# Kernel optimization log

Hardware: AMD Instinct MI355X
Metric: run time of the kernel (lower is better)

Reference implementation:

```python
import jax, jax.numpy as jnp
import numpy as np

EPS = 1e-12  # matches torch F.normalize eps
TEMPERATURE = 1.0


def _l2_normalize(x):
    n = jnp.sqrt(jnp.sum(x * x, axis=-1, keepdims=True))
    return x / jnp.maximum(n, EPS)


def setup_inputs() -> dict:
    key = jax.random.key(0)
    k1, k2 = jax.random.split(key)
    B, L, D, V = 2, 2048, 1024, 32000
    embeddings = jax.random.normal(k1, (B, L, D), dtype=jnp.float32)
    vocab_embeddings = jax.random.normal(k2, (V, D), dtype=jnp.float32)
    return {"embeddings": embeddings, "vocab_embeddings": vocab_embeddings, "k": 8}


def reference(embeddings, vocab_embeddings, k):
    """Soft KNN routing: cosine similarity -> top-k -> temperature softmax
    scattered into a full (B, L, V) probability distribution, plus hard
    argmax token ids (forward())."""
    B, L, D = embeddings.shape
    V = vocab_embeddings.shape[0]
    q = _l2_normalize(embeddings.reshape(-1, D))          # (N, D)
    vocab = _l2_normalize(vocab_embeddings)               # (V, D)
    sims = q @ vocab.T                                    # (N, V) cosine similarities
    topk_sim, topk_idx = jax.lax.top_k(sims, k)           # (N, k)
    probs_k = jax.nn.softmax(topk_sim / TEMPERATURE, axis=-1)
    N = q.shape[0]
    probs = jnp.zeros((N, V), dtype=probs_k.dtype)
    probs = probs.at[jnp.arange(N)[:, None], topk_idx].set(probs_k)
    probs = probs.reshape(B, L, V)                        # forward_soft output
    token_ids = topk_idx[:, 0].reshape(B, L)              # forward() hard routing (k=1)
    return probs, token_ids
```

## Files before the change

### kernel.cpp

```cpp
#include <hip/hip_runtime.h>
#include <math.h>

typedef unsigned short u16;
typedef unsigned int u32;
typedef float f32x16 __attribute__((ext_vector_type(16)));
typedef short bf16x8 __attribute__((ext_vector_type(8)));
typedef u16 u16x4 __attribute__((ext_vector_type(4)));

static constexpr int N = 4096;
static constexpr int D = 1024;
static constexpr int V = 32000;
static constexpr int K = 8;
static constexpr int BM = 128, BN = 128, BK = 64;
static constexpr int NTILES = V / BN;
static constexpr int NG = 32;
static constexpr int NCAND = NG * K;
static constexpr int T16 = 16;
static constexpr int CPL = NCAND / 64;
static constexpr int GRID = NG * (N / BM);
static constexpr u32 PSENT = 0x00800000u;

static constexpr size_t OUT_PROB_BYTES = (size_t)N * V * 4;
static constexpr size_t CAND_OFS = 83886080;
static constexpr size_t ZOFS = CAND_OFS + (size_t)N * NCAND * 4;
static constexpr size_t NZ4 = (OUT_PROB_BYTES - ZOFS) / 16;

static_assert(N % BM == 0 && V % BN == 0, "tiling");
static_assert(ZOFS % 16 == 0, "align");
static_assert(NZ4 == (size_t)104 * GRID * 256, "zero quota");

__device__ __forceinline__ u16 f2bf(float f) {
  u32 u = __float_as_uint(f);
  return (u16)((u + 0x7fffu + ((u >> 16) & 1u)) >> 16);
}
__device__ __forceinline__ u32 flipbits(float v) {
  u32 u = __float_as_uint(v);
  return u ^ (((u32)((int)u >> 31)) | 0x80000000u);
}
__device__ __forceinline__ float unpackval(u32 p) {
  u32 s = p | 1023u;
  u32 u = (s & 0x80000000u) ? (s ^ 0x80000000u) : ~s;
  return __uint_as_float(u);
}
__device__ __forceinline__ void insert8(u32 pv[K], u32 x) {
  if (x <= pv[K - 1]) return;
  bool g[K];
#pragma unroll
  for (int j = 0; j < K; ++j) g[j] = x > pv[j];
#pragma unroll
  for (int j = K - 1; j >= 1; --j)
    pv[j] = g[j - 1] ? pv[j - 1] : (g[j] ? x : pv[j]);
  if (g[0]) pv[0] = x;
}

__global__ void zero_kernel(float4* __restrict__ p, int n4) {
  int i = blockIdx.x * blockDim.x + threadIdx.x;
  int stride = gridDim.x * blockDim.x;
  float4 z = make_float4(0.f, 0.f, 0.f, 0.f);
  for (; i < n4; i += stride) p[i] = z;
}

__global__ void normcvt_kernel(const float* __restrict__ x, float* __restrict__ inv,
                               u16* __restrict__ o) {
  int row = blockIdx.x;
  const float4* xr = reinterpret_cast<const float4*>(x + (size_t)row * D);
  float4 v = xr[threadIdx.x];
  float ss = v.x * v.x + v.y * v.y + v.z * v.z + v.w * v.w;
#pragma unroll
  for (int off = 32; off > 0; off >>= 1) ss += __shfl_down(ss, off, 64);
  __shared__ float wsum[4];
  if ((threadIdx.x & 63) == 0) wsum[threadIdx.x >> 6] = ss;
  __syncthreads();
  __shared__ float s_inv;
  if (threadIdx.x == 0) {
    float t = wsum[0] + wsum[1] + wsum[2] + wsum[3];
    float iv = 1.0f / fmaxf(sqrtf(t), 1e-12f);
    inv[row] = iv;
    s_inv = iv;
  }
  __syncthreads();
  float s = s_inv;
  u16x4 r;
  r[0] = f2bf(v.x * s); r[1] = f2bf(v.y * s); r[2] = f2bf(v.z * s); r[3] = f2bf(v.w * s);
  *reinterpret_cast<u16x4*>(o + (size_t)row * D + threadIdx.x * 4) = r;
}

__global__ __launch_bounds__(256, 4)
void simtopk_kernel(const u16* __restrict__ qn, const u16* __restrict__ vn,
                    u32* __restrict__ cand, float4* __restrict__ zout) {
  __shared__ __align__(16) u16 sh[2 * BM * BK];

  u16* a_sh = sh;
  u16* b_sh = sh + BM * BK;

  const int tid = threadIdx.x;
  const int bid = blockIdx.x;
  const int u = bid >> 3;
  const int rb = u & 31;
  const int grp = (bid & 7) * 4 + (u >> 5);
  const int t0 = (grp * NTILES) >> 5;
  const int t1 = ((grp + 1) * NTILES) >> 5;
  const int rbase = rb * BM;
  const int wid = tid >> 6, l = tid & 63;
  const int wr = wid >> 1, wc = wid & 1;
  const int h = l >> 5, lid = l & 31;
  const int sr = l >> 3;
  const int sk = (((l & 7) ^ (l >> 3)) << 3);

  const float4 zf4 = make_float4(0.f, 0.f, 0.f, 0.f);

  u32 pv[2][K];
#pragma unroll
  for (int n = 0; n < 2; ++n)
#pragma unroll
    for (int j = 0; j < K; ++j) pv[n][j] = PSENT;
  float tminf[2] = {-3.0e38f, -3.0e38f};

  for (int ti = t0; ti < t1; ++ti) {
    const int cb = (ti - t0) * BN;
    f32x16 acc[2][2];
#pragma unroll
    for (int m = 0; m < 2; ++m)
#pragma unroll
      for (int n = 0; n < 2; ++n)
#pragma unroll
        for (int r = 0; r < 16; ++r) acc[m][n][r] = 0.f;

    for (int kk = 0; kk < D / BK; ++kk) {
      __syncthreads();
      {
        int it = (ti - t0) * 16 + kk;
        size_t g = (size_t)it * (GRID * 256) + (size_t)bid * 256 + tid;
        if (g < NZ4) zout[g] = zf4;
      }
      const int kbase = kk * BK;
#pragma unroll
      for (int c = 0; c < 4; ++c) {
        int r = wid * 32 + c * 8 + sr;
        const u16* gs = qn + (size_t)(rbase + r) * D + kbase + sk;
        __builtin_amdgcn_global_load_lds((const __attribute__((address_space(1))) void*)gs,
            (__attribute__((address_space(3))) void*)(a_sh + wid * 2048 + c * 512), 16, 0, 0);
      }
#pragma unroll
      for (int c = 0; c < 4; ++c) {
        int r = wid * 32 + c * 8 + sr;
        const u16* gs = vn + (size_t)(ti * BN + r) * D + kbase + sk;
        __builtin_amdgcn_global_load_lds((const __attribute__((address_space(1))) void*)gs,
            (__attribute__((address_space(3))) void*)(b_sh + wid * 2048 + c * 512), 16, 0, 0);
      }
      __syncthreads();
      __builtin_amdgcn_s_setprio(1);
#pragma unroll
      for (int t = 0; t < 4; ++t) {
        const int ch = t * 2 + h;
        bf16x8 vf[2], qf[2];
#pragma unroll
        for (int m = 0; m < 2; ++m) {
          int row = wr * 64 + m * 32 + lid;
          vf[m] = *reinterpret_cast<const bf16x8*>(b_sh + row * BK + ((ch ^ (row & 7)) << 3));
        }
#pragma unroll
        for (int n = 0; n < 2; ++n) {
          int row = wc * 64 + n * 32 + lid;
          qf[n] = *reinterpret_cast<const bf16x8*>(a_sh + row * BK + ((ch ^ (row & 7)) << 3));
        }
#pragma unroll
        for (int m = 0; m < 2; ++m)
#pragma unroll
          for (int n = 0; n < 2; ++n)
            acc[m][n] = __builtin_amdgcn_mfma_f32_32x32x16_bf16(vf[m], qf[n], acc[m][n], 0, 0, 0);
      }
      __builtin_amdgcn_s_setprio(0);
    }

#pragma unroll
    for (int n = 0; n < 2; ++n) {
#pragma unroll
      for (int m = 0; m < 2; ++m) {
        f32x16 a = acc[m][n];
        float x01 = fmaxf(a[0], a[1]),   x23 = fmaxf(a[2], a[3]);
        float x45 = fmaxf(a[4], a[5]),   x67 = fmaxf(a[6], a[7]);
        float x89 = fmaxf(a[8], a[9]),   xab = fmaxf(a[10], a[11]);
        float xcd = fmaxf(a[12], a[13]), xef = fmaxf(a[14], a[15]);
        float mx = fmaxf(fmaxf(fmaxf(x01, x23), fmaxf(x45, x67)),
                         fmaxf(fmaxf(x89, xab), fmaxf(xcd, xef)));
        if (mx > tminf[n]) {
          const int cidb = cb + wr * 64 + m * 32 + 4 * h;
#pragma unroll
          for (int r = 0; r < 16; ++r) {
            float v = a[r];
            if (v > tminf[n]) {
              int cid = cidb + (r & 3) + 8 * (r >> 2);
              u32 p = (flipbits(v) & 0xFFFFFC00u) | (u32)(1023 - cid);
              insert8(pv[n], p);
            }
          }
          tminf[n] = unpackval(pv[n][K - 1]);
        }
      }
    }
  }

  __syncthreads();
  u32* marr = (u32*)sh;
#pragma unroll
  for (int n = 0; n < 2; ++n)
#pragma unroll
    for (int j = 0; j < K; ++j)
      marr[((wc * 64 + n * 32 + lid) * 4 + (wr * 2 + h)) * K + j] = pv[n][j];
  __syncthreads();
  if (tid < BM) {
    u32 fv[K];
#pragma unroll
    for (int j = 0; j < K; ++j) fv[j] = PSENT;
#pragma unroll
    for (int c4 = 0; c4 < 4; ++c4)
#pragma unroll
      for (int j = 0; j < K; ++j) insert8(fv, marr[(tid * 4 + c4) * K + j]);
#pragma unroll
    for (int j = 0; j < K; ++j)
      cand[(size_t)(rbase + tid) * NCAND + grp * K + j] = fv[j];
  }
}

__global__ __launch_bounds__(256)
void rescore_kernel(const u32* __restrict__ cand,
                    const float* __restrict__ emb, const float* __restrict__ vocab,
                    const float* __restrict__ invq, const float* __restrict__ invv,
                    float* __restrict__ res_p, int* __restrict__ res_i) {
  const int tid = threadIdx.x, wid = tid >> 6, l = tid & 63;
  const int row = blockIdx.x * 4 + wid;

  float4 q[4];
#pragma unroll
  for (int t = 0; t < 4; ++t)
    q[t] = *(reinterpret_cast<const float4*>(emb + (size_t)row * D) + t * 64 + l);
  float iqr = invq[row];

  u32 pl[CPL]; int li[CPL];
#pragma unroll
  for (int t = 0; t < CPL; ++t) {
    int e = l * CPL + t;
    u32 p = cand[(size_t)row * NCAND + e];
    int grp = e >> 3;
    int tile0 = (grp * NTILES) >> 5;
    pl[t] = p;
    li[t] = tile0 * BN + 1023 - (int)(p & 1023u);
  }

  int cidx[T16];
#pragma unroll
  for (int jr = 0; jr < T16; ++jr) {
    u32 bp = pl[0]; int bi = li[0];
#pragma unroll
    for (int t = 1; t < CPL; ++t)
      if (pl[t] > bp || (pl[t] == bp && li[t] < bi)) { bp = pl[t]; bi = li[t]; }
#pragma unroll
    for (int off = 32; off > 0; off >>= 1) {
      u32 op = (u32)__shfl_xor((int)bp, off, 64); int oi = __shfl_xor(bi, off, 64);
      if (op > bp || (op == bp && oi < bi)) { bp = op; bi = oi; }
    }
    cidx[jr] = bi;
#pragma unroll
    for (int t = 0; t < CPL; ++t) if (li[t] == bi) pl[t] = 0u;
  }

  float sv[T16];
#pragma unroll
  for (int jr = 0; jr < T16; ++jr) {
    int ix = cidx[jr];
    const float4* vr = reinterpret_cast<const float4*>(vocab + (size_t)ix * D);
    float s = 0.f;
#pragma unroll
    for (int t = 0; t < 4; ++t) {
      float4 vv = vr[t * 64 + l];
      s += q[t].x * vv.x + q[t].y * vv.y + q[t].z * vv.z + q[t].w * vv.w;
    }
#pragma unroll
    for (int off = 32; off > 0; off >>= 1) s += __shfl_xor(s, off, 64);
    sv[jr] = s * iqr * invv[ix];
  }

  float pvv[K]; int pii[K];
#pragma unroll
  for (int r8 = 0; r8 < K; ++r8) {
    float bv = sv[0]; int bi = cidx[0];
#pragma unroll
    for (int jr = 1; jr < T16; ++jr)
      if (sv[jr] > bv || (sv[jr] == bv && cidx[jr] < bi)) { bv = sv[jr]; bi = cidx[jr]; }
    pvv[r8] = bv; pii[r8] = bi;
#pragma unroll
    for (int jr = 0; jr < T16; ++jr) if (cidx[jr] == bi) sv[jr] = -3.0e38f;
  }

  float m = pvv[0], sum = 0.f, e8[K];
#pragma unroll
  for (int j = 0; j < K; ++j) { e8[j] = expf(pvv[j] - m); sum += e8[j]; }
  float isum = 1.f / sum;
  if (l == 0) {
#pragma unroll
    for (int j = 0; j < K; ++j) {
      res_p[row * K + j] = e8[j] * isum;
      res_i[row * K + j] = pii[j];
    }
  }
}

__global__ void scatter_kernel(const float* __restrict__ res_p, const int* __restrict__ res_i,
                               float* __restrict__ out) {
  int row = blockIdx.x * blockDim.x + threadIdx.x;
#pragma unroll
  for (int j = 0; j < K; ++j) out[(size_t)row * V + res_i[row * K + j]] = res_p[row * K + j];
  out[(size_t)N * V + row] = (float)res_i[row * K];
}

extern "C" void kernel_launch(void* const* d_in, const int* in_sizes, int n_in,
                              void* d_out, int out_size, void* d_ws, size_t ws_size,
                              hipStream_t stream) {
  const float* emb   = (const float*)d_in[0];
  const float* vocab = (const float*)d_in[1];
  float* out = (float*)d_out;

  u16* qn = (u16*)d_out;
  u16* vn = qn + (size_t)N * D;
  u32* cand = (u32*)((char*)d_out + CAND_OFS);
  float4* ztail = (float4*)((char*)d_out + ZOFS);

  float* wsf   = (float*)d_ws;
  float* invq  = wsf;
  float* invv  = wsf + N;
  float* res_p = wsf + N + V;
  int*   res_i = (int*)(wsf + N + V + N * K);

  normcvt_kernel<<<N, 256, 0, stream>>>(emb, invq, qn);
  normcvt_kernel<<<V, 256, 0, stream>>>(vocab, invv, vn);
  simtopk_kernel<<<GRID, 256, 0, stream>>>(qn, vn, cand, ztail);
  rescore_kernel<<<N / 4, 256, 0, stream>>>(cand, emb, vocab, invq, invv, res_p, res_i);
  zero_kernel<<<2048, 256, 0, stream>>>((float4*)d_out, (int)(ZOFS / 16));
  scatter_kernel<<<N / 256, 256, 0, stream>>>(res_p, res_i, out);
}
```

Measured before the change: 535.8 us.

## Triple-buffer K-loop with async LDS loads and batch zero-fill per tile

```diff
diff --git a/kernel.cpp b/kernel.cpp
--- a/kernel.cpp
+++ b/kernel.cpp
@@ -11,7 +11,7 @@
 static constexpr int D = 1024;
 static constexpr int V = 32000;
 static constexpr int K = 8;
-static constexpr int BM = 128, BN = 128, BK = 64;
+static constexpr int BM = 128, BN = 128;
 static constexpr int NTILES = V / BN;
 static constexpr int NG = 32;
 static constexpr int NCAND = NG * K;
@@ -27,7 +27,8 @@
 
 static_assert(N % BM == 0 && V % BN == 0, "tiling");
 static_assert(ZOFS % 16 == 0, "align");
-static_assert(NZ4 == (size_t)104 * GRID * 256, "zero quota");
+static_assert((size_t)32 * 250 * 14 * 256 >= NZ4, "zero quota");
+static_assert((size_t)32 * 250 * 14 * 256 - NZ4 < NZ4, "single wrap");
 
 __device__ __forceinline__ u16 f2bf(float f) {
   u32 u = __float_as_uint(f);
@@ -85,27 +86,26 @@
   *reinterpret_cast<u16x4*>(o + (size_t)row * D + threadIdx.x * 4) = r;
 }
 
-__global__ __launch_bounds__(256, 4)
+__global__ __launch_bounds__(256, 3)
 void simtopk_kernel(const u16* __restrict__ qn, const u16* __restrict__ vn,
                     u32* __restrict__ cand, float4* __restrict__ zout) {
-  __shared__ __align__(16) u16 sh[2 * BM * BK];
-
-  u16* a_sh = sh;
-  u16* b_sh = sh + BM * BK;
+  __shared__ __align__(16) u16 sh[3 * 8192];
 
   const int tid = threadIdx.x;
   const int bid = blockIdx.x;
-  const int u = bid >> 3;
-  const int rb = u & 31;
-  const int grp = (bid & 7) * 4 + (u >> 5);
+  const int u_ = bid >> 3;
+  const int rb = u_ & 31;
+  const int grp = (bid & 7) * 4 + (u_ >> 5);
   const int t0 = (grp * NTILES) >> 5;
   const int t1 = ((grp + 1) * NTILES) >> 5;
+  const int U = (t1 - t0) * 32;
   const int rbase = rb * BM;
   const int wid = tid >> 6, l = tid & 63;
   const int wr = wid >> 1, wc = wid & 1;
   const int h = l >> 5, lid = l & 31;
-  const int sr = l >> 3;
-  const int sk = (((l & 7) ^ (l >> 3)) << 3);
+  const int sc = (((tid & 3) ^ ((tid >> 3) & 3)) << 3);
+  const int sr0 = tid >> 2;
+  const int fsw = (lid >> 1) & 3;
 
   const float4 zf4 = make_float4(0.f, 0.f, 0.f, 0.f);
 
@@ -116,63 +116,59 @@
     for (int j = 0; j < K; ++j) pv[n][j] = PSENT;
   float tminf[2] = {-3.0e38f, -3.0e38f};
 
-  for (int ti = t0; ti < t1; ++ti) {
-    const int cb = (ti - t0) * BN;
-    f32x16 acc[2][2];
-#pragma unroll
-    for (int m = 0; m < 2; ++m)
-#pragma unroll
-      for (int n = 0; n < 2; ++n)
-#pragma unroll
-        for (int r = 0; r < 16; ++r) acc[m][n][r] = 0.f;
-
-    for (int kk = 0; kk < D / BK; ++kk) {
-      __syncthreads();
-      {
-        int it = (ti - t0) * 16 + kk;
-        size_t g = (size_t)it * (GRID * 256) + (size_t)bid * 256 + tid;
-        if (g < NZ4) zout[g] = zf4;
+  f32x16 acc[2][2];
+#pragma unroll
+  for (int m = 0; m < 2; ++m)
+#pragma unroll
+    for (int n = 0; n < 2; ++n)
+#pragma unroll
+      for (int r = 0; r < 16; ++r) acc[m][n][r] = 0.f;
+
+  auto STAGE = [&](int w, int slot) {
+    const int ti = t0 + (w >> 5);
+    const int gk = (w & 31) * 32;
+    u16* ub = sh + slot * 8192;
+#pragma unroll
+    for (int s = 0; s < 2; ++s) {
+      int r = s * 64 + sr0;
+      const u16* gq = qn + (size_t)(rbase + r) * D + gk + sc;
+      __builtin_amdgcn_global_load_lds((const __attribute__((address_space(1))) void*)gq,
+          (__attribute__((address_space(3))) void*)(ub + s * 2048 + wid * 512), 16, 0, 0);
+      const u16* gv = vn + (size_t)(ti * BN + r) * D + gk + sc;
+      __builtin_amdgcn_global_load_lds((const __attribute__((address_space(1))) void*)gv,
+          (__attribute__((address_space(3))) void*)(ub + 4096 + s * 2048 + wid * 512), 16, 0, 0);
+    }
+  };
+
+  auto COMPUTE = [&](int slot) {
+    u16* ub = sh + slot * 8192;
+    __builtin_amdgcn_s_setprio(1);
+#pragma unroll
+    for (int t = 0; t < 2; ++t) {
+      const int ch = t * 2 + h;
+      const int co = (ch ^ fsw) << 3;
+      bf16x8 vf[2], qf[2];
+#pragma unroll
+      for (int m = 0; m < 2; ++m) {
+        int row = wr * 64 + m * 32 + lid;
+        vf[m] = *reinterpret_cast<const bf16x8*>(ub + 4096 + row * 32 + co);
       }
-      const int kbase = kk * BK;
-#pragma unroll
-      for (int c = 0; c < 4; ++c) {
-        int r = wid * 32 + c * 8 + sr;
-        const u16* gs = qn + (size_t)(rbase + r) * D + kbase + sk;
-        __builtin_amdgcn_global_load_lds((const __attribute__((address_space(1))) void*)gs,
-            (__attribute__((address_space(3))) void*)(a_sh + wid * 2048 + c * 512), 16, 0, 0);
+#pragma unroll
+      for (int n = 0; n < 2; ++n) {
+        int row = wc * 64 + n * 32 + lid;
+        qf[n] = *reinterpret_cast<const bf16x8*>(ub + row * 32 + co);
       }
 #pragma unroll
-      for (int c = 0; c < 4; ++c) {
-        int r = wid * 32 + c * 8 + sr;
-        const u16* gs = vn + (size_t)(ti * BN + r) * D + kbase + sk;
-        __builtin_amdgcn_global_load_lds((const __attribute__((address_space(1))) void*)gs,
-            (__attribute__((address_space(3))) void*)(b_sh + wid * 2048 + c * 512), 16, 0, 0);
-      }
-      __syncthreads();
-      __builtin_amdgcn_s_setprio(1);
-#pragma unroll
-      for (int t = 0; t < 4; ++t) {
-        const int ch = t * 2 + h;
-        bf16x8 vf[2], qf[2];
-#pragma unroll
-        for (int m = 0; m < 2; ++m) {
-          int row = wr * 64 + m * 32 + lid;
-          vf[m] = *reinterpret_cast<const bf16x8*>(b_sh + row * BK + ((ch ^ (row & 7)) << 3));
-        }
-#pragma unroll
-        for (int n = 0; n < 2; ++n) {
-          int row = wc * 64 + n * 32 + lid;
-          qf[n] = *reinterpret_cast<const bf16x8*>(a_sh + row * BK + ((ch ^ (row & 7)) << 3));
-        }
-#pragma unroll
-        for (int m = 0; m < 2; ++m)
-#pragma unroll
-          for (int n = 0; n < 2; ++n)
-            acc[m][n] = __builtin_amdgcn_mfma_f32_32x32x16_bf16(vf[m], qf[n], acc[m][n], 0, 0, 0);
-      }
-      __builtin_amdgcn_s_setprio(0);
-    }
-
+      for (int m = 0; m < 2; ++m)
+#pragma unroll
+        for (int n = 0; n < 2; ++n)
+          acc[m][n] = __builtin_amdgcn_mfma_f32_32x32x16_bf16(vf[m], qf[n], acc[m][n], 0, 0, 0);
+    }
+    __builtin_amdgcn_s_setprio(0);
+  };
+
+  auto SCAN = [&](int tt) {
+    const int cb = tt * BN;
 #pragma unroll
     for (int n = 0; n < 2; ++n) {
 #pragma unroll
@@ -199,6 +195,37 @@
         }
       }
     }
+#pragma unroll
+    for (int m = 0; m < 2; ++m)
+#pragma unroll
+      for (int n = 0; n < 2; ++n)
+#pragma unroll
+        for (int r = 0; r < 16; ++r) acc[m][n][r] = 0.f;
+  };
+
+  STAGE(0, 0);
+  STAGE(1, 1);
+  for (int w = 0; w < U; ++w) {
+    const int slot = w % 3;
+    if (w == U - 1)                        asm volatile("s_waitcnt vmcnt(0)" ::: "memory");
+    else if (w >= 32 && (w & 31) <= 1)     asm volatile("s_waitcnt vmcnt(18)" ::: "memory");
+    else                                   asm volatile("s_waitcnt vmcnt(4)" ::: "memory");
+    __builtin_amdgcn_s_barrier();
+    __builtin_amdgcn_sched_barrier(0);
+    if (w + 2 < U) STAGE(w + 2, (w + 2) % 3);
+    COMPUTE(slot);
+    asm volatile("s_waitcnt lgkmcnt(0)" ::: "memory");
+    __builtin_amdgcn_sched_barrier(0);
+    if ((w & 31) == 31) {
+      const int ti = t0 + (w >> 5);
+      size_t gbase = ((size_t)(rb * NTILES + ti) * 14) * 256 + tid;
+#pragma unroll
+      for (int j = 0; j < 14; ++j) {
+        size_t g = gbase + (size_t)j * 256;
+        zout[g < NZ4 ? g : g - NZ4] = zf4;
+      }
+      SCAN(w >> 5);
+    }
   }
 
   __syncthreads();
```

Result: slower. 606.0 us (+13.1%).

## Widen vocab tile to 256 and halve the vocab group count in simtopk

Applied to the files above, without the earlier changes.

```diff
diff --git a/kernel.cpp b/kernel.cpp
--- a/kernel.cpp
+++ b/kernel.cpp
@@ -11,13 +11,15 @@
 static constexpr int D = 1024;
 static constexpr int V = 32000;
 static constexpr int K = 8;
-static constexpr int BM = 128, BN = 128, BK = 64;
-static constexpr int NTILES = V / BN;
-static constexpr int NG = 32;
+static constexpr int BM = 128;
+static constexpr int BV = 256;
+static constexpr int BK = 64;
+static constexpr int NTILES = V / BV;
+static constexpr int NG = 16;
 static constexpr int NCAND = NG * K;
 static constexpr int T16 = 16;
 static constexpr int CPL = NCAND / 64;
-static constexpr int GRID = NG * (N / BM);
+static constexpr int GRID = (N / BM) * NG;
 static constexpr u32 PSENT = 0x00800000u;
 
 static constexpr size_t OUT_PROB_BYTES = (size_t)N * V * 4;
@@ -25,9 +27,9 @@
 static constexpr size_t ZOFS = CAND_OFS + (size_t)N * NCAND * 4;
 static constexpr size_t NZ4 = (OUT_PROB_BYTES - ZOFS) / 16;
 
-static_assert(N % BM == 0 && V % BN == 0, "tiling");
+static_assert(N % BM == 0 && V % BV == 0, "tiling");
 static_assert(ZOFS % 16 == 0, "align");
-static_assert(NZ4 == (size_t)104 * GRID * 256, "zero quota");
+static_assert(NZ4 == (size_t)209 * GRID * 256, "zero quota exact");
 
 __device__ __forceinline__ u16 f2bf(float f) {
   u32 u = __float_as_uint(f);
@@ -38,7 +40,7 @@
   return u ^ (((u32)((int)u >> 31)) | 0x80000000u);
 }
 __device__ __forceinline__ float unpackval(u32 p) {
-  u32 s = p | 1023u;
+  u32 s = p | 2047u;
   u32 u = (s & 0x80000000u) ? (s ^ 0x80000000u) : ~s;
   return __uint_as_float(u);
 }
@@ -85,26 +87,25 @@
   *reinterpret_cast<u16x4*>(o + (size_t)row * D + threadIdx.x * 4) = r;
 }
 
-__global__ __launch_bounds__(256, 4)
+__global__ __launch_bounds__(256, 2)
 void simtopk_kernel(const u16* __restrict__ qn, const u16* __restrict__ vn,
                     u32* __restrict__ cand, float4* __restrict__ zout) {
-  __shared__ __align__(16) u16 sh[2 * BM * BK];
-
-  u16* a_sh = sh;
-  u16* b_sh = sh + BM * BK;
+  __shared__ __align__(16) u16 sh[(BV + BM) * BK];
+
+  u16* v_sh = sh;
+  u16* q_sh = sh + BV * BK;
 
   const int tid = threadIdx.x;
   const int bid = blockIdx.x;
-  const int u = bid >> 3;
-  const int rb = u & 31;
-  const int grp = (bid & 7) * 4 + (u >> 5);
-  const int t0 = (grp * NTILES) >> 5;
-  const int t1 = ((grp + 1) * NTILES) >> 5;
+  const int u_ = bid >> 3;
+  const int rb = u_ & 31;
+  const int grp = (bid & 7) * 2 + (u_ >> 5);
+  const int t0 = (grp * NTILES) >> 4;
+  const int t1 = ((grp + 1) * NTILES) >> 4;
   const int rbase = rb * BM;
   const int wid = tid >> 6, l = tid & 63;
-  const int wr = wid >> 1, wc = wid & 1;
+  const int wv = wid >> 1, wq = wid & 1;
   const int h = l >> 5, lid = l & 31;
-  const int sr = l >> 3;
   const int sk = (((l & 7) ^ (l >> 3)) << 3);
 
   const float4 zf4 = make_float4(0.f, 0.f, 0.f, 0.f);
@@ -117,10 +118,10 @@
   float tminf[2] = {-3.0e38f, -3.0e38f};
 
   for (int ti = t0; ti < t1; ++ti) {
-    const int cb = (ti - t0) * BN;
-    f32x16 acc[2][2];
-#pragma unroll
-    for (int m = 0; m < 2; ++m)
+    const int cb = (ti - t0) * BV;
+    f32x16 acc[4][2];
+#pragma unroll
+    for (int m = 0; m < 4; ++m)
 #pragma unroll
       for (int n = 0; n < 2; ++n)
 #pragma unroll
@@ -130,42 +131,47 @@
       __syncthreads();
       {
         int it = (ti - t0) * 16 + kk;
-        size_t g = (size_t)it * (GRID * 256) + (size_t)bid * 256 + tid;
-        if (g < NZ4) zout[g] = zf4;
+#pragma unroll
+        for (int j = 0; j < 2; ++j) {
+          int s = it * 2 + j;
+          if (s < 209) zout[(size_t)s * (GRID * 256) + bid * 256 + tid] = zf4;
+        }
       }
       const int kbase = kk * BK;
 #pragma unroll
+      for (int c = 0; c < 8; ++c) {
+        int seg = c * 4 + wid;
+        int vrow = seg * 8 + (l >> 3);
+        const u16* gs = vn + (size_t)(ti * BV + vrow) * D + kbase + sk;
+        __builtin_amdgcn_global_load_lds((const __attribute__((address_space(1))) void*)gs,
+            (__attribute__((address_space(3))) void*)(v_sh + seg * 512), 16, 0, 0);
+      }
+#pragma unroll
       for (int c = 0; c < 4; ++c) {
-        int r = wid * 32 + c * 8 + sr;
-        const u16* gs = qn + (size_t)(rbase + r) * D + kbase + sk;
+        int seg = c * 4 + wid;
+        int qrow = seg * 8 + (l >> 3);
+        const u16* gs = qn + (size_t)(rbase + qrow) * D + kbase + sk;
         __builtin_amdgcn_global_load_lds((const __attribute__((address_space(1))) void*)gs,
-            (__attribute__((address_space(3))) void*)(a_sh + wid * 2048 + c * 512), 16, 0, 0);
-      }
-#pragma unroll
-      for (int c = 0; c < 4; ++c) {
-        int r = wid * 32 + c * 8 + sr;
-        const u16* gs = vn + (size_t)(ti * BN + r) * D + kbase + sk;
-        __builtin_amdgcn_global_load_lds((const __attribute__((address_space(1))) void*)gs,
-            (__attribute__((address_space(3))) void*)(b_sh + wid * 2048 + c * 512), 16, 0, 0);
+            (__attribute__((address_space(3))) void*)(q_sh + seg * 512), 16, 0, 0);
       }
       __syncthreads();
       __builtin_amdgcn_s_setprio(1);
 #pragma unroll
       for (int t = 0; t < 4; ++t) {
         const int ch = t * 2 + h;
-        bf16x8 vf[2], qf[2];
-#pragma unroll
-        for (int m = 0; m < 2; ++m) {
-          int row = wr * 64 + m * 32 + lid;
-          vf[m] = *reinterpret_cast<const bf16x8*>(b_sh + row * BK + ((ch ^ (row & 7)) << 3));
+        bf16x8 vf[4], qf[2];
+#pragma unroll
+        for (int m = 0; m < 4; ++m) {
+          int row = wv * 128 + m * 32 + lid;
+          vf[m] = *reinterpret_cast<const bf16x8*>(v_sh + row * BK + ((ch ^ (row & 7)) << 3));
         }
 #pragma unroll
         for (int n = 0; n < 2; ++n) {
-          int row = wc * 64 + n * 32 + lid;
-          qf[n] = *reinterpret_cast<const bf16x8*>(a_sh + row * BK + ((ch ^ (row & 7)) << 3));
+          int row = wq * 64 + n * 32 + lid;
+          qf[n] = *reinterpret_cast<const bf16x8*>(q_sh + row * BK + ((ch ^ (row & 7)) << 3));
         }
 #pragma unroll
-        for (int m = 0; m < 2; ++m)
+        for (int m = 0; m < 4; ++m)
 #pragma unroll
           for (int n = 0; n < 2; ++n)
             acc[m][n] = __builtin_amdgcn_mfma_f32_32x32x16_bf16(vf[m], qf[n], acc[m][n], 0, 0, 0);
@@ -176,7 +182,7 @@
 #pragma unroll
     for (int n = 0; n < 2; ++n) {
 #pragma unroll
-      for (int m = 0; m < 2; ++m) {
+      for (int m = 0; m < 4; ++m) {
         f32x16 a = acc[m][n];
         float x01 = fmaxf(a[0], a[1]),   x23 = fmaxf(a[2], a[3]);
         float x45 = fmaxf(a[4], a[5]),   x67 = fmaxf(a[6], a[7]);
@@ -185,13 +191,13 @@
         float mx = fmaxf(fmaxf(fmaxf(x01, x23), fmaxf(x45, x67)),
                          fmaxf(fmaxf(x89, xab), fmaxf(xcd, xef)));
         if (mx > tminf[n]) {
-          const int cidb = cb + wr * 64 + m * 32 + 4 * h;
+          const int cidb = cb + wv * 128 + m * 32 + 4 * h;
 #pragma unroll
           for (int r = 0; r < 16; ++r) {
             float v = a[r];
             if (v > tminf[n]) {
               int cid = cidb + (r & 3) + 8 * (r >> 2);
-              u32 p = (flipbits(v) & 0xFFFFFC00u) | (u32)(1023 - cid);
+              u32 p = (flipbits(v) & 0xFFFFF800u) | (u32)(2047 - cid);
               insert8(pv[n], p);
             }
           }
@@ -207,7 +213,7 @@
   for (int n = 0; n < 2; ++n)
 #pragma unroll
     for (int j = 0; j < K; ++j)
-      marr[((wc * 64 + n * 32 + lid) * 4 + (wr * 2 + h)) * K + j] = pv[n][j];
+      marr[((wq * 64 + n * 32 + lid) * 4 + (wv * 2 + h)) * K + j] = pv[n][j];
   __syncthreads();
   if (tid < BM) {
     u32 fv[K];
@@ -243,9 +249,9 @@
     int e = l * CPL + t;
     u32 p = cand[(size_t)row * NCAND + e];
     int grp = e >> 3;
-    int tile0 = (grp * NTILES) >> 5;
+    int tile0 = (grp * NTILES) >> 4;
     pl[t] = p;
-    li[t] = tile0 * BN + 1023 - (int)(p & 1023u);
+    li[t] = tile0 * BV + 2047 - (int)(p & 2047u);
   }
 
   int cidx[T16];
```

Measured after the change: 519.4 us. 3.1% less time.
